# Kernel optimization log

Hardware: AMD Instinct MI355X
Metric: run time of the kernel (lower is better)

Reference implementation:

```python
import jax, jax.numpy as jnp
import numpy as np

H = 8
HD = 128
D = 1024
SCALE = 0.12
EOT = 50256
LN_EPS = 1e-6
THETA = 1024.0


def _layernorm(x, w):
    mu = jnp.mean(x, axis=-1, keepdims=True)
    var = jnp.mean(jnp.square(x - mu), axis=-1, keepdims=True)
    return (x - mu) * jax.lax.rsqrt(var + LN_EPS) * w


def _rmsnorm(x):
    eps = jnp.finfo(x.dtype).eps
    return x * jax.lax.rsqrt(jnp.mean(jnp.square(x), axis=-1, keepdims=True) + eps)


def _rope_tables(seq_len, head_dim):
    # half-truncated RoPE: only first half of the rotation pairs get nonzero freqs
    n = head_dim // 4
    freqs = (1.0 / THETA) ** jnp.linspace(0.0, 1.0, n)
    ang = jnp.concatenate([freqs, jnp.zeros((n,), freqs.dtype)])  # [head_dim//2]
    th = jnp.arange(seq_len, dtype=jnp.float32)[:, None] * ang[None, :]
    return jnp.cos(th), jnp.sin(th)  # each [S, head_dim//2]


def _apply_rope(x, cos, sin):
    # x: [B, S, H, hd]
    x1, x2 = jnp.split(x, 2, axis=-1)
    c = cos[None, :, None, :]
    s = sin[None, :, None, :]
    return jnp.concatenate([x1 * c + x2 * s, -x1 * s + x2 * c], axis=-1)


def setup_inputs() -> dict:
    key = jax.random.key(0)
    ks = jax.random.split(key, 10)
    B, S = 2, 2048
    return {
        "x": jax.random.normal(ks[0], (B, S, D), jnp.float32),
        "value_embed": jax.random.normal(ks[1], (S, D), jnp.float32),
        "x0": jax.random.normal(ks[2], (B, S, D), jnp.float32),
        "lambdas": jax.random.uniform(ks[3], (2,), jnp.float32),
        "sa_lambdas": jax.random.uniform(ks[4], (2,), jnp.float32),
        "ln1_w": jnp.ones((D,), jnp.float32),
        "ln2_w": jnp.ones((D,), jnp.float32),
        "w_qkv": jax.random.normal(ks[5], (D, 3 * D), jnp.float32) * 0.02,
        "w_o": jax.random.normal(ks[6], (D, D), jnp.float32) * 0.02,
        "w_fc": jax.random.normal(ks[7], (D, 4 * D), jnp.float32) * 0.02,
        "w_proj": jax.random.normal(ks[8], (4 * D, D), jnp.float32) * 0.02,
        "input_ids": jax.random.randint(ks[9], (S,), 0, 50257, jnp.int64),
    }


def reference(x, value_embed, x0, lambdas, sa_lambdas, ln1_w, ln2_w,
              w_qkv, w_o, w_fc, w_proj, input_ids):
    B, S, Dm = x.shape
    # U-Net residual mixing
    x = lambdas[0] * x + lambdas[1] * x0

    # attention branch
    xn = _layernorm(x, ln1_w)
    qkv = xn @ w_qkv                                # [B,S,3D]
    q, k, v = jnp.split(qkv, 3, axis=-1)
    q = q.reshape(B, S, H, HD)
    k = k.reshape(B, S, H, HD)
    v = v.reshape(B, S, H, HD)

    cos, sin = _rope_tables(S, HD)
    q = _apply_rope(q, cos, sin)
    k = _apply_rope(k, cos, sin)

    # value-embedding mixing
    ve = value_embed.reshape(S, H, HD)[None]        # [1,S,H,hd]
    v = sa_lambdas[0] * v + sa_lambdas[1] * ve

    # QK norm (unit-weight RMSNorm)
    q = _rmsnorm(q)
    k = _rmsnorm(k)

    # document-aware causal mask
    docs = jnp.cumsum(input_ids == EOT)
    idx = jnp.arange(S)
    mask = (idx[:, None] >= idx[None, :]) & (docs[:, None] == docs[None, :])

    scores = jnp.einsum("bqhd,bkhd->bhqk", q, k) * SCALE
    scores = jnp.where(mask[None, None], scores, -jnp.inf)
    attn = jax.nn.softmax(scores, axis=-1)
    out = jnp.einsum("bhqk,bkhd->bqhd", attn, v).reshape(B, S, Dm)
    x = x + out @ w_o

    # MLP with relu^2
    xn = _layernorm(x, ln2_w)
    h = jnp.square(jax.nn.relu(xn @ w_fc))
    x = x + h @ w_proj
    return x
```

## Files before the change

### kernel.cpp

```cpp
#include <hip/hip_runtime.h>

#define EOT_ID 50256

typedef __attribute__((ext_vector_type(8))) short bf16x8;
typedef __attribute__((ext_vector_type(4))) float f32x4;
typedef __attribute__((ext_vector_type(16))) float f32x16;

#define GLOAD_LDS(g, l)                                                        \
  __builtin_amdgcn_global_load_lds(                                            \
      (const __attribute__((address_space(1))) unsigned int*)(g),              \
      (__attribute__((address_space(3))) unsigned int*)(l), 16, 0, 0)

__device__ __forceinline__ unsigned short f2bf(float f) {
  union { float f; unsigned int u; } v; v.f = f;
  unsigned int r = v.u + 0x7FFFu + ((v.u >> 16) & 1u);
  return (unsigned short)(r >> 16);
}
__device__ __forceinline__ float bf2f(unsigned short b) {
  union { unsigned int u; float f; } v; v.u = ((unsigned int)b) << 16;
  return v.f;
}
__device__ __forceinline__ unsigned int cvtpk(float lo, float hi) {
  unsigned int r;
  asm("v_cvt_pk_bf16_f32 %0, %1, %2" : "=v"(r) : "v"(lo), "v"(hi));
  return r;
}
__device__ __forceinline__ void plswap(unsigned int& a, unsigned int& b) {
  asm volatile("v_permlane32_swap_b32 %0, %1" : "+v"(a), "+v"(b));
}
union U8 { unsigned int u[4]; bf16x8 v; };

__global__ void rope_tab_kernel(float* __restrict__ ct, float* __restrict__ st) {
  const int idx = blockIdx.x * 256 + threadIdx.x;
  const int s = idx >> 5, i = idx & 31;
  const float ang = (float)s * exp2f(-10.0f * (float)i / 31.0f);
  float sv, cv;
  sincosf(ang, &sv, &cv);
  ct[idx] = cv;
  st[idx] = sv;
}

__global__ __launch_bounds__(1024)
void docs_kernel(const int* __restrict__ ids, int* __restrict__ qstart) {
  __shared__ int a[2048], b2[2048];
  const int t = threadIdx.x;
  for (int i = t; i < 2048; i += 1024)
    a[i] = (ids[i] == EOT_ID) ? i : 0;
  __syncthreads();
  int* cur = a; int* nxt = b2;
  for (int off = 1; off < 2048; off <<= 1) {
    for (int i = t; i < 2048; i += 1024) {
      int v = cur[i];
      if (i >= off) { int u = cur[i - off]; v = (u > v) ? u : v; }
      nxt[i] = v;
    }
    __syncthreads();
    int* tmp = cur; cur = nxt; nxt = tmp;
  }
  for (int i = t; i < 2048; i += 1024) qstart[i] = cur[i];
}

__global__ __launch_bounds__(256)
void wtrans_kernel(const float* __restrict__ in, unsigned short* __restrict__ out,
                   int K, int N) {
  __shared__ float tile[32][33];
  const int nb = N >> 5;
  const int k0 = (blockIdx.x / nb) << 5, n0 = (blockIdx.x % nb) << 5;
  const int tx = threadIdx.x & 31, ty = threadIdx.x >> 5;
#pragma unroll
  for (int p = 0; p < 4; p++)
    tile[ty + p * 8][tx] = in[(size_t)(k0 + ty + p * 8) * N + n0 + tx];
  __syncthreads();
#pragma unroll
  for (int p = 0; p < 4; p++)
    out[(size_t)(n0 + ty + p * 8) * K + k0 + tx] = f2bf(tile[tx][ty + p * 8]);
}

template<bool MIX>
__global__ __launch_bounds__(256)
void ln_kernel(const float* __restrict__ x, const float* __restrict__ x0,
               const float* __restrict__ lam, const float* __restrict__ w,
               float* __restrict__ xm, unsigned short* __restrict__ xn) {
  __shared__ float red[8];
  const int row = blockIdx.x, t = threadIdx.x;
  const size_t base = (size_t)row << 10;
  float4 v = *(const float4*)(x + base + t * 4);
  if (MIX) {
    const float l0 = lam[0], l1 = lam[1];
    const float4 v0 = *(const float4*)(x0 + base + t * 4);
    v.x = l0 * v.x + l1 * v0.x;
    v.y = l0 * v.y + l1 * v0.y;
    v.z = l0 * v.z + l1 * v0.z;
    v.w = l0 * v.w + l1 * v0.w;
    *(float4*)(xm + base + t * 4) = v;
  }
  float s = v.x + v.y + v.z + v.w;
  float q = v.x * v.x + v.y * v.y + v.z * v.z + v.w * v.w;
#pragma unroll
  for (int off = 1; off < 64; off <<= 1) {
    s += __shfl_xor(s, off);
    q += __shfl_xor(q, off);
  }
  const int wid = t >> 6;
  if ((t & 63) == 0) { red[wid] = s; red[4 + wid] = q; }
  __syncthreads();
  s = red[0] + red[1] + red[2] + red[3];
  q = red[4] + red[5] + red[6] + red[7];
  const float mu = s * (1.0f / 1024.0f);
  const float var = q * (1.0f / 1024.0f) - mu * mu;
  const float rstd = rsqrtf(var + 1e-6f);
  const float4 wv = *(const float4*)(w + t * 4);
  ushort4 u;
  u.x = f2bf((v.x - mu) * rstd * wv.x);
  u.y = f2bf((v.y - mu) * rstd * wv.y);
  u.z = f2bf((v.z - mu) * rstd * wv.z);
  u.w = f2bf((v.w - mu) * rstd * wv.w);
  *(ushort4*)(xn + base + t * 4) = u;
}

template<int EPI, int BM, int BK>
__global__ __launch_bounds__(256, 4)
void gemm_bt(const unsigned short* __restrict__ A,
             const unsigned short* __restrict__ Bt,
             void* __restrict__ Cout,
             const float* __restrict__ res,
             int M, int N, int K) {
  __shared__ unsigned short As[2][BM * BK];
  __shared__ unsigned short Bs[2][128 * BK];
  const int t = threadIdx.x;
  const int wid = t >> 6;
  const int lane = t & 63;
  const int ln = lane & 15, kg = lane >> 4;
  const int nbm = M / BM;
  const int xcd = (int)blockIdx.x & 7, rr = (int)blockIdx.x >> 3;
  const int slab = nbm >> 3;
  const int bm = xcd * slab + (rr % slab);
  const int bn = rr / slab;
  const int m0 = bm * BM, n0 = bn << 7;
  const int wrow = (BM == 128) ? ((wid >> 1) * 64) : 0;
  const int wcol = (BM == 128) ? ((wid & 1) * 64) : (wid * 32);
  constexpr int NJ = (BM == 128) ? 4 : 2;
  constexpr int LA = BM * BK / 2048;
  constexpr int LB = 128 * BK / 2048;
  constexpr int KC = BK / 32;

  f32x4 acc[4][NJ] = {};

  const unsigned short* Abase = A + (size_t)m0 * K;
  const unsigned short* Bbase = Bt + (size_t)n0 * K;

  auto swz = [&](int row, int chunk) -> int {
    if constexpr (BK == 32) return chunk ^ ((row >> 1) & 3);
    else                    return chunk ^ (row & 7);
  };

  auto STAGE = [&](int bb, int kt) {
#pragma unroll
    for (int p = 0; p < LA; p++) {
      const int e = t * 8 + p * 2048;
      const int r = e / BK;
      const int cs = swz(r, (e >> 3) & (BK / 8 - 1));
      GLOAD_LDS(Abase + (size_t)r * K + kt + cs * 8, &As[bb][p * 2048 + wid * 512]);
    }
#pragma unroll
    for (int p = 0; p < LB; p++) {
      const int e = t * 8 + p * 2048;
      const int r = e / BK;
      const int cs = swz(r, (e >> 3) & (BK / 8 - 1));
      GLOAD_LDS(Bbase + (size_t)r * K + kt + cs * 8, &Bs[bb][p * 2048 + wid * 512]);
    }
  };

  STAGE(0, 0);
  int cur = 0;
  const int nk = K / BK;
  for (int ki = 0; ki < nk; ki++) {
    if (ki + 1 < nk) {
      STAGE(cur ^ 1, (ki + 1) * BK);
      if constexpr (LA + LB == 4)
        asm volatile("s_waitcnt vmcnt(4)" ::: "memory");
      else
        asm volatile("s_waitcnt vmcnt(6)" ::: "memory");
    } else {
      asm volatile("s_waitcnt vmcnt(0)" ::: "memory");
    }
    __builtin_amdgcn_s_barrier();

#pragma unroll
    for (int c = 0; c < KC; c++) {
      bf16x8 af[4], bfr[NJ];
#pragma unroll
      for (int i = 0; i < 4; i++) {
        const int ra = wrow + i * 16 + ln;
        af[i] = *(const bf16x8*)(&As[cur][ra * BK + swz(ra, c * 4 + kg) * 8]);
      }
#pragma unroll
      for (int j = 0; j < NJ; j++) {
        const int rb = wcol + j * 16 + ln;
        bfr[j] = *(const bf16x8*)(&Bs[cur][rb * BK + swz(rb, c * 4 + kg) * 8]);
      }
#pragma unroll
      for (int i = 0; i < 4; i++)
#pragma unroll
        for (int j = 0; j < NJ; j++)
          acc[i][j] = __builtin_amdgcn_mfma_f32_16x16x32_bf16(af[i], bfr[j], acc[i][j], 0, 0, 0);
    }

    __builtin_amdgcn_s_barrier();
    cur ^= 1;
  }

#pragma unroll
  for (int i = 0; i < 4; i++) {
#pragma unroll
    for (int j = 0; j < NJ; j++) {
#pragma unroll
      for (int r = 0; r < 4; r++) {
        const int row = m0 + wrow + i * 16 + kg * 4 + r;
        const int col = n0 + wcol + j * 16 + ln;
        const size_t idx = (size_t)row * N + col;
        float v = acc[i][j][r];
        if (EPI == 0) {
          ((float*)Cout)[idx] = v;
        } else if (EPI == 1) {
          ((float*)Cout)[idx] = v + res[idx];
        } else if (EPI == 2) {
          v = fmaxf(v, 0.0f);
          ((unsigned short*)Cout)[idx] = f2bf(v * v);
        } else {
          ((unsigned short*)Cout)[idx] = f2bf(v);
        }
      }
    }
  }
}

#define SWZ9(x) ((x) ^ ((((x) >> 9) & 1) << 5))

#define RD_A(BUF, QM)                                                          \
  {                                                                            \
    const char* sb_ = smem + (((BUF)*2 + 0) * 2 + (QM)) * 16384;               \
    _Pragma("unroll") for (int i_ = 0; i_ < 4; i_++)                           \
    _Pragma("unroll") for (int kc_ = 0; kc_ < 2; kc_++) {                      \
      int x_ = kc_ * 8192 + (wr * 64 + i_ * 16 + ln) * 64 + kg * 16;           \
      Af[i_][kc_] = *(const bf16x8*)(sb_ + SWZ9(x_));                          \
    }                                                                          \
  }

#define RD_B(BUF, QN, BARR)                                                    \
  {                                                                            \
    const char* sb_ = smem + (((BUF)*2 + 1) * 2 + (QN)) * 16384;               \
    _Pragma("unroll") for (int j_ = 0; j_ < 2; j_++)                           \
    _Pragma("unroll") for (int kc_ = 0; kc_ < 2; kc_++) {                      \
      int x_ = kc_ * 8192 + (wc * 32 + j_ * 16 + ln) * 64 + kg * 16;           \
      BARR[j_][kc_] = *(const bf16x8*)(sb_ + SWZ9(x_));                        \
    }                                                                          \
  }

#define MFMAQ(QM, QN, BARR)                                                    \
  _Pragma("unroll") for (int i_ = 0; i_ < 4; i_++)                             \
  _Pragma("unroll") for (int j_ = 0; j_ < 2; j_++)                             \
  _Pragma("unroll") for (int kc_ = 0; kc_ < 2; kc_++)                          \
    acc[QM][QN][i_][j_] = __builtin_amdgcn_mfma_f32_16x16x32_bf16(             \
        Af[i_][kc_], BARR[j_][kc_], acc[QM][QN][i_][j_], 0, 0, 0);

#define PHTAIL()                                                               \
  __builtin_amdgcn_s_barrier();                                                \
  asm volatile("s_waitcnt lgkmcnt(0)" ::: "memory");                           \
  __builtin_amdgcn_sched_barrier(0);                                           \
  __builtin_amdgcn_s_setprio(1)

#define PHEND()                                                                \
  __builtin_amdgcn_s_setprio(0);                                               \
  __builtin_amdgcn_s_barrier()

template<int EPI>
__global__ __launch_bounds__(512, 2)
void gemm256(const unsigned short* __restrict__ A,
             const unsigned short* __restrict__ Bt,
             void* __restrict__ Cout,
             int M, int N, int K) {
  extern __shared__ char smem[];
  const int tid = threadIdx.x;
  const int wid = tid >> 6, lane = tid & 63;
  const int wr = wid >> 2, wc = wid & 3;
  const int ln = lane & 15, kg = lane >> 4;
  const int nbm = M >> 8;
  const int xcd = (int)blockIdx.x & 7, rr = (int)blockIdx.x >> 3;
  const int slab = nbm >> 3;
  const int bm = xcd * slab + (rr % slab);
  const int bn = rr / slab;
  const int m0 = bm << 8, n0 = bn << 8;
  const size_t K2 = (size_t)K * 2;
  const char* Ac = (const char*)A;
  const char* Bc = (const char*)Bt;

  f32x4 acc[2][2][4][2] = {};
  bf16x8 Af[4][2], B0[2][2], B1[2][2];

  auto STG = [&](int buf, int ab, int h, int tile) {
    const char* gb = ab ? Bc : Ac;
    const int ro = (ab ? n0 : m0) + h * 128;
    char* db = smem + ((buf * 2 + ab) * 2 + h) * 16384;
#pragma unroll
    for (int q = 0; q < 2; q++) {
      const int p0 = q * 8192 + tid * 16;
      const int lin = SWZ9(p0);
      GLOAD_LDS(gb + (size_t)(ro + ((lin >> 6) & 127)) * K2 +
                    (size_t)tile * 128 + (lin >> 13) * 64 + (lin & 63),
                db + p0);
    }
  };

  STG(0, 0, 0, 0); STG(0, 0, 1, 0); STG(0, 1, 0, 0); STG(0, 1, 1, 0);
  STG(1, 0, 0, 1); STG(1, 1, 0, 1); STG(1, 1, 1, 1);
  asm volatile("s_waitcnt vmcnt(6)" ::: "memory");
  __builtin_amdgcn_s_barrier();

  const int niter = K >> 7;
  for (int it = 0; it < niter; it++) {
    const int tA = 2 * it, tB = tA + 1;
    const bool more = (it + 1 < niter);

    RD_A(0, 0); RD_B(0, 0, B0);
    STG(1, 0, 1, tB);
    PHTAIL(); MFMAQ(0, 0, B0); PHEND();
    RD_B(0, 1, B1);
    if (more) STG(0, 0, 0, tA + 2);
    PHTAIL(); MFMAQ(0, 1, B1); PHEND();
    RD_A(0, 1);
    if (more) STG(0, 1, 0, tA + 2);
    PHTAIL(); MFMAQ(1, 0, B0); PHEND();
    if (more) {
      STG(0, 1, 1, tA + 2);
      asm volatile("s_waitcnt vmcnt(6)" ::: "memory");
    } else {
      asm volatile("s_waitcnt vmcnt(0)" ::: "memory");
    }
    PHTAIL(); MFMAQ(1, 1, B1); PHEND();
    RD_A(1, 0); RD_B(1, 0, B0);
    if (more) STG(0, 0, 1, tA + 2);
    PHTAIL(); MFMAQ(0, 0, B0); PHEND();
    RD_B(1, 1, B1);
    if (more) STG(1, 0, 0, tB + 2);
    PHTAIL(); MFMAQ(0, 1, B1); PHEND();
    RD_A(1, 1);
    if (more) STG(1, 1, 0, tB + 2);
    PHTAIL(); MFMAQ(1, 0, B0); PHEND();
    if (more) {
      STG(1, 1, 1, tB + 2);
      asm volatile("s_waitcnt vmcnt(6)" ::: "memory");
    }
    PHTAIL(); MFMAQ(1, 1, B1); PHEND();
  }

#pragma unroll
  for (int qm = 0; qm < 2; qm++)
#pragma unroll
    for (int qn = 0; qn < 2; qn++)
#pragma unroll
      for (int i = 0; i < 4; i++)
#pragma unroll
        for (int j = 0; j < 2; j++)
#pragma unroll
          for (int r = 0; r < 4; r++) {
            const int row = m0 + qm * 128 + wr * 64 + i * 16 + kg * 4 + r;
            const int col = n0 + qn * 128 + wc * 32 + j * 16 + ln;
            const size_t idx = (size_t)row * N + col;
            float v = acc[qm][qn][i][j][r];
            if (EPI == 2) {
              v = fmaxf(v, 0.0f);
              ((unsigned short*)Cout)[idx] = f2bf(v * v);
            } else {
              ((unsigned short*)Cout)[idx] = f2bf(v);
            }
          }
}

__global__ __launch_bounds__(256)
void rope_rms_kernel(const unsigned short* __restrict__ qkv,
                     const float* __restrict__ ct, const float* __restrict__ st,
                     const float* __restrict__ ve, const float* __restrict__ salam,
                     unsigned short* __restrict__ Qh, unsigned short* __restrict__ Kh,
                     unsigned short* __restrict__ Vt) {
  const int t = threadIdx.x;
  const int wid = t >> 6, i = t & 63;
  const int g = blockIdx.x * 4 + wid;
  const int b = g >> 14;
  const int s = (g >> 3) & 2047;
  const int h = g & 7;
  const unsigned short* base = qkv + (size_t)(b * 2048 + s) * 3072 + h * 128;
  float c = 1.0f, sn = 0.0f;
  if (i < 32) { c = ct[s * 32 + i]; sn = st[s * 32 + i]; }
  const float q1 = bf2f(base[i]), q2 = bf2f(base[64 + i]);
  const float k1 = bf2f(base[1024 + i]), k2 = bf2f(base[1024 + 64 + i]);
  const float q1r = q1 * c + q2 * sn, q2r = q2 * c - q1 * sn;
  const float k1r = k1 * c + k2 * sn, k2r = k2 * c - k1 * sn;
  float sq = q1r * q1r + q2r * q2r;
  float sk = k1r * k1r + k2r * k2r;
#pragma unroll
  for (int off = 1; off < 64; off <<= 1) {
    sq += __shfl_xor(sq, off);
    sk += __shfl_xor(sk, off);
  }
  const float eps = 1.1920929e-7f;
  const float rq = rsqrtf(sq * (1.0f / 128.0f) + eps);
  const float rk = rsqrtf(sk * (1.0f / 128.0f) + eps);
  unsigned short* qp = Qh + (((size_t)(b * 2048 + s) * 8 + h) << 7);
  unsigned short* kp = Kh + (((size_t)(b * 2048 + s) * 8 + h) << 7);
  qp[i] = f2bf(q1r * rq); qp[64 + i] = f2bf(q2r * rq);
  kp[i] = f2bf(k1r * rk); kp[64 + i] = f2bf(k2r * rk);
  const float l0 = salam[0], l1 = salam[1];
  const float* vep = ve + (size_t)s * 1024 + h * 128;
  const float v1 = l0 * bf2f(base[2048 + i]) + l1 * vep[i];
  const float v2 = l0 * bf2f(base[2048 + 64 + i]) + l1 * vep[64 + i];
  unsigned short* vp = Vt + (((size_t)(b * 8 + h) * 128) << 11) + s;
  vp[(size_t)i << 11] = f2bf(v1);
  vp[(size_t)(64 + i) << 11] = f2bf(v2);
}

__global__ __launch_bounds__(512, 2)
void attn_kernel(const unsigned short* __restrict__ Qh,
                 const unsigned short* __restrict__ Kh,
                 const unsigned short* __restrict__ Vt,
                 const int* __restrict__ qstart,
                 unsigned short* __restrict__ Out) {
  extern __shared__ char asmem[];

  const int blk = blockIdx.x;
  const int pid = blk >> 4;
  const int bh = blk & 15;
  const int b = bh >> 3, h = bh & 7;
  const int t = threadIdx.x;
  const int wid = t >> 6, lane = t & 63;
  const int qw = wid & 1, kw = wid >> 1;
  const int ln5 = lane & 31, hi = lane >> 5;
  const int tp = qw * 64 + lane;
  const float SC = 0.12f * 1.4426950408889634f;

  unsigned short* Kb = (unsigned short*)(asmem + kw * 16384);
  unsigned short* Vb = (unsigned short*)(asmem + 65536 + kw * 16384);

  auto STAGE = [&](int bb, int kt) {
#pragma unroll
    for (int r = 0; r < 4; r++) {
      const int e = tp * 16 + r * 2048;
      const int row = e >> 8;
      const int ch = (e >> 4) & 15;
      const int sch = ch ^ ((row ^ (row >> 3)) & 7);
      GLOAD_LDS(Kh + (((size_t)(b * 2048 + kt + row) * 8 + h) << 7) + sch * 8,
                (char*)Kb + bb * 8192 + r * 2048 + qw * 1024 + (lane << 4));
    }
#pragma unroll
    for (int r = 0; r < 4; r++) {
      const int e = tp * 16 + r * 2048;
      const int row = e >> 6;
      const int ch = (e >> 4) & 3;
      const int sch = ch ^ ((row >> 1) & 3);
      GLOAD_LDS(Vt + (((size_t)((b * 8 + h) * 128 + row)) << 11) + kt + sch * 8,
                (char*)Vb + bb * 8192 + r * 2048 + qw * 1024 + (lane << 4));
    }
  };

  for (int ph = 0; ph < 2; ph++) {
    const int qt = ph ? (31 - pid) : pid;
    const int q0 = qt << 6;
    const int qrow = q0 + qw * 32;

    bf16x8 qf[8];
    {
      const unsigned short* qp =
          Qh + (((size_t)(b * 2048 + qrow + ln5) * 8 + h) << 7) + hi * 8;
#pragma unroll
      for (int c = 0; c < 8; c++) qf[c] = *(const bf16x8*)(qp + c * 16);
    }
    const int qid = qrow + ln5;
    const int qs = qstart[qid];
    int qsmax = qs;
#pragma unroll
    for (int off = 1; off < 32; off <<= 1)
      qsmax = max(qsmax, __shfl_xor(qsmax, off));

    float m = -64.0f, l = 0.0f;
    f32x16 o[4] = {};

    const int kt0 = qstart[q0] & ~31;
    const int T = (q0 + 64 - kt0) >> 5;

    __syncthreads();
    STAGE(0, kt0 + kw * 32);
    int cur = 0;
    const int nLoop = (T + 3) >> 2;

    for (int i = 0; i < nLoop; i++) {
      const int tid2 = 4 * i + kw;
      const bool hasnext = (tid2 + 4) < T;
      if (hasnext) {
        STAGE(cur ^ 1, kt0 + (tid2 + 4) * 32);
        asm volatile("s_waitcnt vmcnt(8)" ::: "memory");
      } else {
        asm volatile("s_waitcnt vmcnt(0)" ::: "memory");
      }
      __builtin_amdgcn_s_barrier();

      if (tid2 < T) {
        const int kt = kt0 + tid2 * 32;
        const unsigned short* ksb = (const unsigned short*)((char*)Kb + cur * 8192);
        const unsigned short* vsb = (const unsigned short*)((char*)Vb + cur * 8192);

        f32x16 sacc = {};
        {
          const int key = ln5;
          const int kx = (key ^ (key >> 3)) & 7;
          const unsigned short* krow = &ksb[key * 128];
#pragma unroll
          for (int c = 0; c < 8; c++) {
            bf16x8 kf = *(const bf16x8*)(krow + (((2 * c + hi) ^ kx) << 3));
            sacc = __builtin_amdgcn_mfma_f32_32x32x16_bf16(kf, qf[c], sacc, 0, 0, 0);
          }
        }

        const bool full = (kt + 32 <= qrow) && (kt >= qsmax);

        float p[16];
        float mx = -1e30f;
        if (full) {
#pragma unroll
          for (int i2 = 0; i2 < 16; i2++) {
            const float ts = sacc[i2] * SC;
            p[i2] = ts;
            mx = fmaxf(mx, ts);
          }
        } else {
#pragma unroll
          for (int i2 = 0; i2 < 16; i2++) {
            const int key = kt + (i2 & 3) + 8 * (i2 >> 2) + 4 * hi;
            const bool valid = (key <= qid) && (key >= qs);
            const float ts = valid ? sacc[i2] * SC : -1e30f;
            p[i2] = ts;
            mx = fmaxf(mx, ts);
          }
        }
        mx = fmaxf(mx, __shfl_xor(mx, 32));

        const bool dresc = __any(mx - m > 8.0f);
        if (dresc) {
          const float mn = fmaxf(m, mx);
          const float fac = exp2f(m - mn);
          m = mn;
          l *= fac;
#pragma unroll
          for (int r = 0; r < 16; r++) {
            const float fr = __shfl(fac, (r & 3) + 8 * (r >> 2) + 4 * hi);
            o[0][r] *= fr; o[1][r] *= fr; o[2][r] *= fr; o[3][r] *= fr;
          }
        }

        float sum = 0.0f;
#pragma unroll
        for (int i2 = 0; i2 < 16; i2++) {
          const float pv = exp2f(p[i2] - m);
          p[i2] = pv;
          sum += pv;
        }
        sum += __shfl_xor(sum, 32);
        l += sum;

        bf16x8 pa[2];
#pragma unroll
        for (int bb2 = 0; bb2 < 2; bb2++) {
          unsigned int a0 = cvtpk(p[bb2 * 8 + 0], p[bb2 * 8 + 1]);
          unsigned int b0 = cvtpk(p[bb2 * 8 + 4], p[bb2 * 8 + 5]);
          unsigned int a1 = cvtpk(p[bb2 * 8 + 2], p[bb2 * 8 + 3]);
          unsigned int b1 = cvtpk(p[bb2 * 8 + 6], p[bb2 * 8 + 7]);
          plswap(a0, b0);
          plswap(a1, b1);
          U8 u; u.u[0] = a0; u.u[1] = a1; u.u[2] = b0; u.u[3] = b1;
          pa[bb2] = u.v;
        }

#pragma unroll
        for (int dt = 0; dt < 4; dt++) {
          const int d = dt * 32 + ln5;
          const int dx = (d >> 1) & 3;
          const unsigned short* vrow = &vsb[d * 32];
#pragma unroll
          for (int ks = 0; ks < 2; ks++) {
            bf16x8 vf = *(const bf16x8*)(vrow + (((2 * ks + hi) ^ dx) << 3));
            o[dt] = __builtin_amdgcn_mfma_f32_32x32x16_bf16(pa[ks], vf, o[dt], 0, 0, 0);
          }
        }
      }

      __builtin_amdgcn_s_barrier();
      cur ^= 1;
    }

    __syncthreads();
    float* oex = (float*)asmem;
    float* mlx = (float*)(asmem + 99840);
    if (kw != 0) {
      if (lane < 32) {
        mlx[(((kw - 1) * 2 + qw) * 32 + lane) * 2 + 0] = m;
        mlx[(((kw - 1) * 2 + qw) * 32 + lane) * 2 + 1] = l;
      }
      float* dst = oex + (((kw - 1) * 2 + qw) * 64 + lane) * 65;
#pragma unroll
      for (int dt = 0; dt < 4; dt++)
#pragma unroll
        for (int r = 0; r < 16; r++) dst[dt * 16 + r] = o[dt][r];
    }
    __syncthreads();
    if (kw == 0) {
      float mm[3], ll[3];
#pragma unroll
      for (int j = 0; j < 3; j++) {
        mm[j] = mlx[((j * 2 + qw) * 32 + ln5) * 2 + 0];
        ll[j] = mlx[((j * 2 + qw) * 32 + ln5) * 2 + 1];
      }
      const float ms = fmaxf(fmaxf(m, mm[0]), fmaxf(mm[1], mm[2]));
      const float a0 = exp2f(m - ms);
      const float a1 = exp2f(mm[0] - ms);
      const float a2 = exp2f(mm[1] - ms);
      const float a3 = exp2f(mm[2] - ms);
      const float inv = 1.0f / (l * a0 + ll[0] * a1 + ll[1] * a2 + ll[2] * a3);
      const float* s1 = oex + ((0 * 2 + qw) * 64 + lane) * 65;
      const float* s2 = oex + ((1 * 2 + qw) * 64 + lane) * 65;
      const float* s3 = oex + ((2 * 2 + qw) * 64 + lane) * 65;
#pragma unroll
      for (int r = 0; r < 16; r++) {
        const int crow = (r & 3) + 8 * (r >> 2) + 4 * hi;
        const float a0r = __shfl(a0, crow);
        const float a1r = __shfl(a1, crow);
        const float a2r = __shfl(a2, crow);
        const float a3r = __shfl(a3, crow);
        const float ivr = __shfl(inv, crow);
        const int q = qrow + crow;
        unsigned short* op = Out + (((size_t)(b * 2048 + q)) << 10) + h * 128 + ln5;
#pragma unroll
        for (int dt = 0; dt < 4; dt++)
          op[dt * 32] = f2bf((o[dt][r] * a0r + s1[dt * 16 + r] * a1r +
                              s2[dt * 16 + r] * a2r + s3[dt * 16 + r] * a3r) * ivr);
      }
    }
  }
}

extern "C" void kernel_launch(void* const* d_in, const int* in_sizes, int n_in,
                              void* d_out, int out_size, void* d_ws, size_t ws_size,
                              hipStream_t stream) {
  const float* x     = (const float*)d_in[0];
  const float* vemb  = (const float*)d_in[1];
  const float* x0    = (const float*)d_in[2];
  const float* lam   = (const float*)d_in[3];
  const float* slam  = (const float*)d_in[4];
  const float* ln1w  = (const float*)d_in[5];
  const float* ln2w  = (const float*)d_in[6];
  const float* wqkv  = (const float*)d_in[7];
  const float* wo    = (const float*)d_in[8];
  const float* wfc   = (const float*)d_in[9];
  const float* wproj = (const float*)d_in[10];
  const int*   ids   = (const int*)d_in[11];

  char* ws = (char*)d_ws;
  unsigned short* wqkvT  = (unsigned short*)(ws + 0);
  unsigned short* woT    = (unsigned short*)(ws + 6291456);
  unsigned short* wfcT   = (unsigned short*)(ws + 8388608);
  unsigned short* wprojT = (unsigned short*)(ws + 16777216);
  float*          xm     = (float*)(ws + 25165824);
  unsigned short* qkv    = (unsigned short*)(ws + 41943040);
  unsigned short* hbuf   = (unsigned short*)(ws + 41943040);
  unsigned short* xn1    = (unsigned short*)(ws + 92274688);
  unsigned short* ao     = (unsigned short*)(ws + 92274688);
  unsigned short* qh     = (unsigned short*)(ws + 100663296);
  unsigned short* xn2    = (unsigned short*)(ws + 100663296);
  unsigned short* kh     = (unsigned short*)(ws + 109051904);
  unsigned short* vt     = (unsigned short*)(ws + 117440512);
  float*          x2     = (float*)(ws + 109051904);
  float*          ctab   = (float*)(ws + 125829120);
  float*          stab   = (float*)(ws + 126091264);
  int*            qstart = (int*)(ws + 126353408);

  static int attr_done = 0;
  if (!attr_done) {
    hipFuncSetAttribute((const void*)gemm256<3>,
                        hipFuncAttributeMaxDynamicSharedMemorySize, 131072);
    hipFuncSetAttribute((const void*)gemm256<2>,
                        hipFuncAttributeMaxDynamicSharedMemorySize, 131072);
    hipFuncSetAttribute((const void*)attn_kernel,
                        hipFuncAttributeMaxDynamicSharedMemorySize, 131072);
    attr_done = 1;
  }

  rope_tab_kernel<<<dim3(256), dim3(256), 0, stream>>>(ctab, stab);
  docs_kernel<<<dim3(1), dim3(1024), 0, stream>>>(ids, qstart);
  wtrans_kernel<<<dim3(32 * 96), dim3(256), 0, stream>>>(wqkv, wqkvT, 1024, 3072);
  wtrans_kernel<<<dim3(32 * 32), dim3(256), 0, stream>>>(wo, woT, 1024, 1024);
  wtrans_kernel<<<dim3(32 * 128), dim3(256), 0, stream>>>(wfc, wfcT, 1024, 4096);
  wtrans_kernel<<<dim3(128 * 32), dim3(256), 0, stream>>>(wproj, wprojT, 4096, 1024);

  ln_kernel<true><<<dim3(4096), dim3(256), 0, stream>>>(x, x0, lam, ln1w, xm, xn1);
  gemm256<3><<<dim3(192), dim3(512), 131072, stream>>>(xn1, wqkvT, (void*)qkv,
                                                       4096, 3072, 1024);
  rope_rms_kernel<<<dim3(8192), dim3(256), 0, stream>>>(qkv, ctab, stab, vemb, slam, qh, kh, vt);
  attn_kernel<<<dim3(256), dim3(512), 131072, stream>>>(qh, kh, vt, qstart, ao);
  gemm_bt<1, 64, 64><<<dim3(64 * 8), dim3(256), 0, stream>>>(ao, woT, (void*)x2, xm,
                                                             4096, 1024, 1024);
  ln_kernel<false><<<dim3(4096), dim3(256), 0, stream>>>(x2, (const float*)nullptr,
                                                         (const float*)nullptr, ln2w,
                                                         (float*)nullptr, xn2);
  gemm256<2><<<dim3(256), dim3(512), 131072, stream>>>(xn2, wfcT, (void*)hbuf,
                                                       4096, 4096, 1024);
  gemm_bt<1, 64, 64><<<dim3(64 * 8), dim3(256), 0, stream>>>(hbuf, wprojT, d_out, x2,
                                                             4096, 1024, 4096);
}
```

Measured before the change: 257.3 us.

## Split-K the MLP down-projection across four partial GEMMs and reduce

The final 4096x1024x4096 projection moves from the small-tile gemm_bt kernel to the 256x256 MFMA gemm256 kernel with a 4-way K split. That gives 256 blocks instead of 64 large-tile ones, and each split writes a bf16 partial buffer. A new add5 kernel then sums the four partials with the fp32 residual into the output. The aim is to use the faster large-tile pipeline while keeping all CUs busy, at the cost of extra partial-buffer traffic, an extra launch, and bf16 rounding of the partial sums.

```diff
diff --git a/kernel.cpp b/kernel.cpp
--- a/kernel.cpp
+++ b/kernel.cpp
@@ -74,6 +74,25 @@
 #pragma unroll
   for (int p = 0; p < 4; p++)
     out[(size_t)(n0 + ty + p * 8) * K + k0 + tx] = f2bf(tile[tx][ty + p * 8]);
+}
+
+__global__ __launch_bounds__(256)
+void add5_kernel(const unsigned short* __restrict__ p0,
+                 const unsigned short* __restrict__ p1,
+                 const unsigned short* __restrict__ p2,
+                 const unsigned short* __restrict__ p3,
+                 const float* __restrict__ res, float* __restrict__ out) {
+  const int i = (blockIdx.x * 256 + threadIdx.x) * 4;
+  const ushort4 a = *(const ushort4*)(p0 + i);
+  const ushort4 b = *(const ushort4*)(p1 + i);
+  const ushort4 c = *(const ushort4*)(p2 + i);
+  const ushort4 d = *(const ushort4*)(p3 + i);
+  float4 e = *(const float4*)(res + i);
+  e.x += bf2f(a.x) + bf2f(b.x) + bf2f(c.x) + bf2f(d.x);
+  e.y += bf2f(a.y) + bf2f(b.y) + bf2f(c.y) + bf2f(d.y);
+  e.z += bf2f(a.z) + bf2f(b.z) + bf2f(c.z) + bf2f(d.z);
+  e.w += bf2f(a.w) + bf2f(b.w) + bf2f(c.w) + bf2f(d.w);
+  *(float4*)(out + i) = e;
 }
 
 template<bool MIX>
@@ -274,24 +293,33 @@
   __builtin_amdgcn_s_setprio(0);                                               \
   __builtin_amdgcn_s_barrier()
 
-template<int EPI>
+template<int EPI, bool KSPLIT4>
 __global__ __launch_bounds__(512, 2)
 void gemm256(const unsigned short* __restrict__ A,
              const unsigned short* __restrict__ Bt,
              void* __restrict__ Cout,
-             int M, int N, int K) {
+             int M, int N, int Kfull, int Klen, int nInner,
+             unsigned short* __restrict__ o1, unsigned short* __restrict__ o2,
+             unsigned short* __restrict__ o3) {
   extern __shared__ char smem[];
   const int tid = threadIdx.x;
   const int wid = tid >> 6, lane = tid & 63;
   const int wr = wid >> 2, wc = wid & 3;
   const int ln = lane & 15, kg = lane >> 4;
+  int blkid = (int)blockIdx.x;
+  int split = 0;
+  if constexpr (KSPLIT4) {
+    split = blkid / nInner;
+    blkid -= split * nInner;
+  }
   const int nbm = M >> 8;
-  const int xcd = (int)blockIdx.x & 7, rr = (int)blockIdx.x >> 3;
+  const int xcd = blkid & 7, rr = blkid >> 3;
   const int slab = nbm >> 3;
   const int bm = xcd * slab + (rr % slab);
   const int bn = rr / slab;
   const int m0 = bm << 8, n0 = bn << 8;
-  const size_t K2 = (size_t)K * 2;
+  const size_t K2 = (size_t)Kfull * 2;
+  const size_t kb0 = (size_t)split * Klen * 2;
   const char* Ac = (const char*)A;
   const char* Bc = (const char*)Bt;
 
@@ -306,7 +334,7 @@
     for (int q = 0; q < 2; q++) {
       const int p0 = q * 8192 + tid * 16;
       const int lin = SWZ9(p0);
-      GLOAD_LDS(gb + (size_t)(ro + ((lin >> 6) & 127)) * K2 +
+      GLOAD_LDS(gb + (size_t)(ro + ((lin >> 6) & 127)) * K2 + kb0 +
                     (size_t)tile * 128 + (lin >> 13) * 64 + (lin & 63),
                 db + p0);
     }
@@ -317,7 +345,7 @@
   asm volatile("s_waitcnt vmcnt(6)" ::: "memory");
   __builtin_amdgcn_s_barrier();
 
-  const int niter = K >> 7;
+  const int niter = Klen >> 7;
   for (int it = 0; it < niter; it++) {
     const int tA = 2 * it, tB = tA + 1;
     const bool more = (it + 1 < niter);
@@ -354,6 +382,13 @@
     PHTAIL(); MFMAQ(1, 1, B1); PHEND();
   }
 
+  unsigned short* bout = (unsigned short*)Cout;
+  if constexpr (KSPLIT4) {
+    if (split == 1) bout = o1;
+    else if (split == 2) bout = o2;
+    else if (split == 3) bout = o3;
+  }
+
 #pragma unroll
   for (int qm = 0; qm < 2; qm++)
 #pragma unroll
@@ -371,8 +406,10 @@
             if (EPI == 2) {
               v = fmaxf(v, 0.0f);
               ((unsigned short*)Cout)[idx] = f2bf(v * v);
+            } else if (EPI == 3) {
+              ((unsigned short*)Cout)[idx] = f2bf(v);
             } else {
-              ((unsigned short*)Cout)[idx] = f2bf(v);
+              bout[idx] = f2bf(v);
             }
           }
 }
@@ -680,12 +717,18 @@
   float*          ctab   = (float*)(ws + 125829120);
   float*          stab   = (float*)(ws + 126091264);
   int*            qstart = (int*)(ws + 126353408);
+  unsigned short* P0 = (unsigned short*)(ws + 0);
+  unsigned short* P1 = (unsigned short*)(ws + 8388608);
+  unsigned short* P2 = (unsigned short*)(ws + 25165824);
+  unsigned short* P3 = (unsigned short*)(ws + 33554432);
 
   static int attr_done = 0;
   if (!attr_done) {
-    hipFuncSetAttribute((const void*)gemm256<3>,
+    hipFuncSetAttribute((const void*)gemm256<3, false>,
                         hipFuncAttributeMaxDynamicSharedMemorySize, 131072);
-    hipFuncSetAttribute((const void*)gemm256<2>,
+    hipFuncSetAttribute((const void*)gemm256<2, false>,
+                        hipFuncAttributeMaxDynamicSharedMemorySize, 131072);
+    hipFuncSetAttribute((const void*)gemm256<4, true>,
                         hipFuncAttributeMaxDynamicSharedMemorySize, 131072);
     hipFuncSetAttribute((const void*)attn_kernel,
                         hipFuncAttributeMaxDynamicSharedMemorySize, 131072);
@@ -700,8 +743,8 @@
   wtrans_kernel<<<dim3(128 * 32), dim3(256), 0, stream>>>(wproj, wprojT, 4096, 1024);
 
   ln_kernel<true><<<dim3(4096), dim3(256), 0, stream>>>(x, x0, lam, ln1w, xm, xn1);
-  gemm256<3><<<dim3(192), dim3(512), 131072, stream>>>(xn1, wqkvT, (void*)qkv,
-                                                       4096, 3072, 1024);
+  gemm256<3, false><<<dim3(192), dim3(512), 131072, stream>>>(
+      xn1, wqkvT, (void*)qkv, 4096, 3072, 1024, 1024, 0, nullptr, nullptr, nullptr);
   rope_rms_kernel<<<dim3(8192), dim3(256), 0, stream>>>(qkv, ctab, stab, vemb, slam, qh, kh, vt);
   attn_kernel<<<dim3(256), dim3(512), 131072, stream>>>(qh, kh, vt, qstart, ao);
   gemm_bt<1, 64, 64><<<dim3(64 * 8), dim3(256), 0, stream>>>(ao, woT, (void*)x2, xm,
@@ -709,8 +752,9 @@
   ln_kernel<false><<<dim3(4096), dim3(256), 0, stream>>>(x2, (const float*)nullptr,
                                                          (const float*)nullptr, ln2w,
                                                          (float*)nullptr, xn2);
-  gemm256<2><<<dim3(256), dim3(512), 131072, stream>>>(xn2, wfcT, (void*)hbuf,
-                                                       4096, 4096, 1024);
-  gemm_bt<1, 64, 64><<<dim3(64 * 8), dim3(256), 0, stream>>>(hbuf, wprojT, d_out, x2,
-                                                             4096, 1024, 4096);
-}
+  gemm256<2, false><<<dim3(256), dim3(512), 131072, stream>>>(
+      xn2, wfcT, (void*)hbuf, 4096, 4096, 1024, 1024, 0, nullptr, nullptr, nullptr);
+  gemm256<4, true><<<dim3(256), dim3(512), 131072, stream>>>(
+      hbuf, wprojT, (void*)P0, 4096, 1024, 4096, 1024, 64, P1, P2, P3);
+  add5_kernel<<<dim3(4096), dim3(256), 0, stream>>>(P0, P1, P2, P3, x2, (float*)d_out);
+}
```

Result: faster. 250.6 us (-2.6%).
